# Kernel optimization log

Measured on AMD Instinct MI355X. Metric: run time of the kernel, lower is better.

Reference implementation:

```python
import jax, jax.numpy as jnp
import numpy as np

EPS = 1e-12  # matches torch F.normalize eps clamp


def _l2norm(v, axis):
    n = jnp.sqrt(jnp.sum(v * v, axis=axis, keepdims=True))
    return v / jnp.maximum(n, EPS)


def setup_inputs() -> dict:
    key = jax.random.key(0)
    k1, k2, k3, k4 = jax.random.split(key, 4)
    N, C, H, W, K = 64, 128, 64, 64, 64
    x = jax.random.normal(k1, (N, C, H, W), dtype=jnp.float32)
    conv_w = jax.random.normal(k2, (K, C), dtype=jnp.float32) * 0.1  # 1x1 conv weight squeezed
    conv_b = jax.random.normal(k3, (K,), dtype=jnp.float32) * 0.1
    centroids = jax.random.uniform(k4, (K, C), dtype=jnp.float32)
    return {"x": x, "conv_w": conv_w, "conv_b": conv_b, "centroids": centroids}


def reference(x, conv_w, conv_b, centroids):
    N, C = x.shape[:2]
    K = centroids.shape[0]
    xf = x.reshape(N, C, -1)                                   # (N, C, P) with P = H*W
    # 1x1 conv == per-pixel linear map over channels
    logits = jnp.einsum('ncp,kc->nkp', xf, conv_w) + conv_b[None, :, None]
    a = jax.nn.softmax(logits, axis=1)                         # soft assignment over clusters
    # vlad[n,k,c] = sum_p a[n,k,p] * (x[n,c,p] - centroids[k,c])
    vlad = jnp.einsum('nkp,ncp->nkc', a, xf) \
        - jnp.sum(a, axis=-1)[:, :, None] * centroids[None]    # (N, K, C)
    vlad = _l2norm(vlad, axis=2)                               # intra-cluster normalization
    vlad = vlad.reshape(N, K * C)
    return _l2norm(vlad, axis=1)
```

## Files before the change

kernel.cpp:

```cpp
#include <hip/hip_runtime.h>
#include <math.h>

#define NNIMG 64
#define CCH 128
#define KK 64
#define PP 4096
#define BSPLIT 16
#define PB (PP / BSPLIT)
#define PC 32
#define NCHUNK (PB / PC)

typedef __attribute__((ext_vector_type(8))) short short8;
typedef __attribute__((ext_vector_type(4))) float f32x4;

__device__ __forceinline__ unsigned short bf16_rtne(float f) {
  unsigned u = __float_as_uint(f);
  unsigned r = u + 0x7FFFu + ((u >> 16) & 1u);
  return (unsigned short)(r >> 16);
}
__device__ __forceinline__ float bf16_tof(unsigned short h) {
  return __uint_as_float(((unsigned)h) << 16);
}
__device__ __forceinline__ void lgkm_barrier() {
  __asm__ volatile("s_waitcnt lgkmcnt(0)\n\ts_barrier" ::: "memory");
}

template <bool USE_WS>
__global__ __launch_bounds__(128, 2) void netvlad_main(
    const float* __restrict__ x, const float* __restrict__ conv_w,
    const float* __restrict__ conv_b, const float* __restrict__ centroids,
    float* __restrict__ vout, float* __restrict__ aout) {
  __shared__ __align__(16) unsigned int pc[2][PC * 66];
  __shared__ __align__(16) unsigned short a_lds[KK * 40];
  __shared__ __align__(16) unsigned short w_lds[16 * 64 * 8];
  __shared__ float asum_buf[2 * KK];

  const int t = threadIdx.x;
  const int lane = t & 63;
  const int wv = t >> 6;
  const int m = lane & 15;
  const int q = lane >> 4;

  const int n = blockIdx.x / BSPLIT;
  const int blk = blockIdx.x % BSPLIT;
  const float* xbase = x + (size_t)n * CCH * PP + blk * PB;

  const int lrow = lane >> 3;
  const int lpx = (lane & 7) * 4;
  f32x4 sregA[8], sregB[8];
  auto issue_loads = [&](int ch, f32x4 (&sr)[8]) {
#pragma unroll
    for (int j = 0; j < 8; ++j) {
      const int row = wv * 64 + (j >> 1) * 16 + lrow * 2 + (j & 1);
      sr[j] = *(const f32x4*)(xbase + (size_t)row * PP + ch * PC + lpx);
    }
  };

  issue_loads(0, sregA);
  issue_loads(1, sregB);

#pragma unroll
  for (int kt = 0; kt < 4; ++kt)
#pragma unroll
    for (int cs = 0; cs < 4; ++cs) {
      const float* wp = conv_w + (kt * 16 + m) * CCH + cs * 32 + q * 8;
      float4 wa = *(const float4*)wp;
      float4 wb = *(const float4*)(wp + 4);
      float fv[8] = {wa.x, wa.y, wa.z, wa.w, wb.x, wb.y, wb.z, wb.w};
      short8 h;
#pragma unroll
      for (int j = 0; j < 8; ++j) h[j] = (short)bf16_rtne(fv[j]);
      *(short8*)&w_lds[(kt * 4 + cs) * 512 + lane * 8] = h;
    }
  float b_regs[4][4];
#pragma unroll
  for (int kt = 0; kt < 4; ++kt)
#pragma unroll
    for (int r = 0; r < 4; ++r) b_regs[kt][r] = conv_b[kt * 16 + q * 4 + r];

  f32x4 vacc[4][4];
#pragma unroll
  for (int kt = 0; kt < 4; ++kt)
#pragma unroll
    for (int ct = 0; ct < 4; ++ct) vacc[kt][ct] = (f32x4){0.f, 0.f, 0.f, 0.f};
  float asum_acc[16];
#pragma unroll
  for (int i = 0; i < 16; ++i) asum_acc[i] = 0.f;

  const int prow = wv * 16 + m;
  const unsigned sel_hi = 0x07060302u;
  const unsigned sel_g2 = (m & 1) ? 0x07060302u : 0x05040100u;

  auto chunk_body = [&](int ch, f32x4 (&sc)[8]) {
    unsigned int* pcb = pc[ch & 1];

#pragma unroll
    for (int u = 0; u < 4; ++u) {
      const int e = wv * 32 + u * 8 + lrow;
      f32x4 ev = sc[2 * u];
      f32x4 od = sc[2 * u + 1];
#pragma unroll
      for (int pi = 0; pi < 4; ++pi)
        pcb[(lpx + pi) * 66 + e] =
            __builtin_amdgcn_perm(__float_as_uint(od[pi]), __float_as_uint(ev[pi]), sel_hi);
    }
    if (ch + 2 < NCHUNK) issue_loads(ch + 2, sc);
    lgkm_barrier();

    f32x4 acc1[4];
#pragma unroll
    for (int kt = 0; kt < 4; ++kt)
      acc1[kt] = (f32x4){b_regs[kt][0], b_regs[kt][1], b_regs[kt][2], b_regs[kt][3]};
    const unsigned int* pcrow = pcb + prow * 66;
#pragma unroll
    for (int cs = 0; cs < 4; ++cs) {
      uint2 u01 = *(const uint2*)&pcrow[16 * cs + 4 * q];
      uint2 u23 = *(const uint2*)&pcrow[16 * cs + 4 * q + 2];
      unsigned hs[4] = {u01.x, u01.y, u23.x, u23.y};
      short8 Bf;
      __builtin_memcpy(&Bf, hs, 16);
#pragma unroll
      for (int kt = 0; kt < 4; ++kt) {
        short8 Wf = *(const short8*)&w_lds[(kt * 4 + cs) * 512 + lane * 8];
        acc1[kt] = __builtin_amdgcn_mfma_f32_16x16x32_bf16(Wf, Bf, acc1[kt], 0, 0, 0);
      }
    }

    float ssum = 0.f;
#pragma unroll
    for (int kt = 0; kt < 4; ++kt)
#pragma unroll
      for (int r = 0; r < 4; ++r) {
        float e = __expf(acc1[kt][r]);
        acc1[kt][r] = e;
        ssum += e;
      }
    ssum += __shfl_xor(ssum, 16, 64);
    ssum += __shfl_xor(ssum, 32, 64);
    float inv = 1.0f / ssum;
#pragma unroll
    for (int kt = 0; kt < 4; ++kt)
#pragma unroll
      for (int r = 0; r < 4; ++r) {
        float a = acc1[kt][r] * inv;
        unsigned short h = bf16_rtne(a);
        asum_acc[kt * 4 + r] += bf16_tof(h);
        a_lds[(kt * 16 + q * 4 + r) * 40 + prow] = h;
      }
    lgkm_barrier();

    short8 Af[4];
#pragma unroll
    for (int kt = 0; kt < 4; ++kt)
      Af[kt] = *(const short8*)&a_lds[(kt * 16 + m) * 40 + q * 8];
#pragma unroll
    for (int ct = 0; ct < 4; ++ct) {
      const int ebase = wv * 32 + ct * 8 + (m >> 1);
      unsigned g[8];
#pragma unroll
      for (int j = 0; j < 8; ++j) g[j] = pcb[(q * 8 + j) * 66 + ebase];
      unsigned hs2[4];
#pragma unroll
      for (int i = 0; i < 4; ++i)
        hs2[i] = __builtin_amdgcn_perm(g[2 * i + 1], g[2 * i], sel_g2);
      short8 Bf;
      __builtin_memcpy(&Bf, hs2, 16);
#pragma unroll
      for (int kt = 0; kt < 4; ++kt)
        vacc[kt][ct] = __builtin_amdgcn_mfma_f32_16x16x32_bf16(Af[kt], Bf, vacc[kt][ct], 0, 0, 0);
    }
  };

#pragma unroll 1
  for (int ch = 0; ch < NCHUNK; ch += 2) {
    chunk_body(ch, sregA);
    chunk_body(ch + 1, sregB);
  }

#pragma unroll
  for (int i = 0; i < 16; ++i) {
    float v = asum_acc[i];
    v += __shfl_xor(v, 1, 64);
    v += __shfl_xor(v, 2, 64);
    v += __shfl_xor(v, 4, 64);
    v += __shfl_xor(v, 8, 64);
    if (m == 0) asum_buf[wv * 64 + (i >> 2) * 16 + q * 4 + (i & 3)] = v;
  }
  lgkm_barrier();

  if (USE_WS) {
    float* vrow = vout + (size_t)blockIdx.x * (KK * CCH);
#pragma unroll
    for (int kt = 0; kt < 4; ++kt)
#pragma unroll
      for (int ct = 0; ct < 4; ++ct)
#pragma unroll
        for (int r = 0; r < 4; ++r) {
          const int idx = (kt * 16 + q * 4 + r) * CCH + wv * 64 + ct * 16 + m;
          vrow[idx] = vacc[kt][ct][r];
        }
    if (t < KK) aout[blockIdx.x * KK + t] = asum_buf[t] + asum_buf[KK + t];
  } else {
    float s_k[16];
#pragma unroll
    for (int i = 0; i < 16; ++i) {
      const int k = (i >> 2) * 16 + q * 4 + (i & 3);
      s_k[i] = asum_buf[k] + asum_buf[KK + k];
    }
    float* orow = vout + (size_t)n * (KK * CCH);
#pragma unroll
    for (int kt = 0; kt < 4; ++kt)
#pragma unroll
      for (int ct = 0; ct < 4; ++ct)
#pragma unroll
        for (int r = 0; r < 4; ++r) {
          const int k = kt * 16 + q * 4 + r;
          const int c = wv * 64 + ct * 16 + m;
          atomicAdd(&orow[k * CCH + c],
                    vacc[kt][ct][r] - s_k[kt * 4 + r] * centroids[k * CCH + c]);
        }
  }
}

__global__ __launch_bounds__(256) void netvlad_finish_ws(
    const float* __restrict__ vp, const float* __restrict__ agp,
    const float* __restrict__ centroids, float* __restrict__ out) {
  const int t = threadIdx.x;
  const int w = t >> 6, ln = t & 63;
  const int idx = blockIdx.x * 4 + w;
  const int n = idx >> 6, k = idx & 63;
  const int c = ln * 2;
  float a0 = 0.f, a1 = 0.f, s = 0.f;
#pragma unroll
  for (int b = 0; b < BSPLIT; ++b) {
    const float* vr = vp + (size_t)(n * BSPLIT + b) * (KK * CCH) + k * CCH + c;
    float2 v = *(const float2*)vr;
    a0 += v.x;
    a1 += v.y;
    s += agp[(n * BSPLIT + b) * KK + k];
  }
  float2 ce = *(const float2*)&centroids[k * CCH + c];
  float v0 = a0 - s * ce.x;
  float v1 = a1 - s * ce.y;
  float ssq = v0 * v0 + v1 * v1;
#pragma unroll
  for (int off = 32; off > 0; off >>= 1) ssq += __shfl_xor(ssq, off, 64);
  float inv = 0.125f / fmaxf(sqrtf(ssq), 1e-12f);
  float2 o;
  o.x = v0 * inv;
  o.y = v1 * inv;
  *(float2*)&out[(size_t)n * (KK * CCH) + k * CCH + c] = o;
}

__global__ __launch_bounds__(256) void netvlad_norm(float* __restrict__ out) {
  const int t = threadIdx.x;
  const int w = t >> 6, ln = t & 63;
  const int idx = blockIdx.x * 4 + w;
  float* vr = out + (size_t)idx * CCH;
  const int c = ln * 2;
  float2 v = *(const float2*)&vr[c];
  float ssq = v.x * v.x + v.y * v.y;
#pragma unroll
  for (int off = 32; off > 0; off >>= 1) ssq += __shfl_xor(ssq, off, 64);
  float inv = 0.125f / fmaxf(sqrtf(ssq), 1e-12f);
  float2 o;
  o.x = v.x * inv;
  o.y = v.y * inv;
  *(float2*)&vr[c] = o;
}

extern "C" void kernel_launch(void* const* d_in, const int* in_sizes, int n_in,
                              void* d_out, int out_size, void* d_ws, size_t ws_size,
                              hipStream_t stream) {
  const float* x = (const float*)d_in[0];
  const float* conv_w = (const float*)d_in[1];
  const float* conv_b = (const float*)d_in[2];
  const float* centroids = (const float*)d_in[3];
  float* out = (float*)d_out;

  const size_t WS_NEEDED =
      ((size_t)NNIMG * BSPLIT * KK * CCH + (size_t)NNIMG * BSPLIT * KK) * sizeof(float);

  if (ws_size >= WS_NEEDED) {
    float* vp = (float*)d_ws;
    float* agp = vp + (size_t)NNIMG * BSPLIT * KK * CCH;
    netvlad_main<true><<<NNIMG * BSPLIT, 128, 0, stream>>>(x, conv_w, conv_b,
                                                           centroids, vp, agp);
    netvlad_finish_ws<<<NNIMG * KK / 4, 256, 0, stream>>>(vp, agp, centroids, out);
  } else {
    hipMemsetAsync(d_out, 0, (size_t)NNIMG * KK * CCH * sizeof(float), stream);
    netvlad_main<false><<<NNIMG * BSPLIT, 128, 0, stream>>>(x, conv_w, conv_b,
                                                            centroids, out, nullptr);
    netvlad_norm<<<NNIMG * KK / 4, 256, 0, stream>>>(out);
  }
}
```

Before: 211.2 us.

## Stage 64-pixel chunks in a single LDS buffer with wider row loads

The x tile is now staged 64 pixels at a time in one LDS buffer instead of two 32-pixel double-buffered chunks, and each chunk is processed as two 32-pixel sub-chunks. The global load pattern changes to 16 lanes spanning 64 contiguous pixels per row, giving 256-byte contiguous row segments instead of 128-byte ones. The prefetch distance is now one 64-pixel chunk instead of two 32-pixel chunks. A single buffer adds an extra barrier after every sub-chunk, and the staging writes can no longer overlap with reads from the previous chunk.

Result: no change. 215.0 us (+1.8%).

```diff
diff --git a/kernel.cpp b/kernel.cpp
--- a/kernel.cpp
+++ b/kernel.cpp
@@ -7,8 +7,8 @@
 #define PP 4096
 #define BSPLIT 16
 #define PB (PP / BSPLIT)
-#define PC 32
-#define NCHUNK (PB / PC)
+#define CPW 64
+#define NCP (PB / CPW)
 
 typedef __attribute__((ext_vector_type(8))) short short8;
 typedef __attribute__((ext_vector_type(4))) float f32x4;
@@ -30,7 +30,7 @@
     const float* __restrict__ x, const float* __restrict__ conv_w,
     const float* __restrict__ conv_b, const float* __restrict__ centroids,
     float* __restrict__ vout, float* __restrict__ aout) {
-  __shared__ __align__(16) unsigned int pc[2][PC * 66];
+  __shared__ __align__(16) unsigned int pc[CPW * 66];
   __shared__ __align__(16) unsigned short a_lds[KK * 40];
   __shared__ __align__(16) unsigned short w_lds[16 * 64 * 8];
   __shared__ float asum_buf[2 * KK];
@@ -45,19 +45,17 @@
   const int blk = blockIdx.x % BSPLIT;
   const float* xbase = x + (size_t)n * CCH * PP + blk * PB;
 
-  const int lrow = lane >> 3;
-  const int lpx = (lane & 7) * 4;
-  f32x4 sregA[8], sregB[8];
-  auto issue_loads = [&](int ch, f32x4 (&sr)[8]) {
-#pragma unroll
-    for (int j = 0; j < 8; ++j) {
-      const int row = wv * 64 + (j >> 1) * 16 + lrow * 2 + (j & 1);
-      sr[j] = *(const f32x4*)(xbase + (size_t)row * PP + ch * PC + lpx);
+  f32x4 sregE[8], sregO[8];
+  auto issue_loads = [&](int cp) {
+#pragma unroll
+    for (int u = 0; u < 8; ++u) {
+      const float* pe = xbase + (size_t)(wv * 64 + u * 8 + 2 * q) * PP + cp * CPW + m * 4;
+      sregE[u] = *(const f32x4*)pe;
+      sregO[u] = *(const f32x4*)(pe + PP);
     }
   };
 
-  issue_loads(0, sregA);
-  issue_loads(1, sregB);
+  issue_loads(0);
 
 #pragma unroll
   for (int kt = 0; kt < 4; ++kt)
@@ -87,94 +85,92 @@
 #pragma unroll
   for (int i = 0; i < 16; ++i) asum_acc[i] = 0.f;
 
-  const int prow = wv * 16 + m;
   const unsigned sel_hi = 0x07060302u;
   const unsigned sel_g2 = (m & 1) ? 0x07060302u : 0x05040100u;
 
-  auto chunk_body = [&](int ch, f32x4 (&sc)[8]) {
-    unsigned int* pcb = pc[ch & 1];
-
-#pragma unroll
-    for (int u = 0; u < 4; ++u) {
-      const int e = wv * 32 + u * 8 + lrow;
-      f32x4 ev = sc[2 * u];
-      f32x4 od = sc[2 * u + 1];
+#pragma unroll 1
+  for (int cp = 0; cp < NCP; ++cp) {
+#pragma unroll
+    for (int u = 0; u < 8; ++u) {
+      const int e = wv * 32 + u * 4 + q;
+      f32x4 ev = sregE[u];
+      f32x4 od = sregO[u];
 #pragma unroll
       for (int pi = 0; pi < 4; ++pi)
-        pcb[(lpx + pi) * 66 + e] =
+        pc[(m * 4 + pi) * 66 + e] =
             __builtin_amdgcn_perm(__float_as_uint(od[pi]), __float_as_uint(ev[pi]), sel_hi);
     }
-    if (ch + 2 < NCHUNK) issue_loads(ch + 2, sc);
+    if (cp + 1 < NCP) issue_loads(cp + 1);
     lgkm_barrier();
 
-    f32x4 acc1[4];
-#pragma unroll
-    for (int kt = 0; kt < 4; ++kt)
-      acc1[kt] = (f32x4){b_regs[kt][0], b_regs[kt][1], b_regs[kt][2], b_regs[kt][3]};
-    const unsigned int* pcrow = pcb + prow * 66;
-#pragma unroll
-    for (int cs = 0; cs < 4; ++cs) {
-      uint2 u01 = *(const uint2*)&pcrow[16 * cs + 4 * q];
-      uint2 u23 = *(const uint2*)&pcrow[16 * cs + 4 * q + 2];
-      unsigned hs[4] = {u01.x, u01.y, u23.x, u23.y};
-      short8 Bf;
-      __builtin_memcpy(&Bf, hs, 16);
-#pragma unroll
-      for (int kt = 0; kt < 4; ++kt) {
-        short8 Wf = *(const short8*)&w_lds[(kt * 4 + cs) * 512 + lane * 8];
-        acc1[kt] = __builtin_amdgcn_mfma_f32_16x16x32_bf16(Wf, Bf, acc1[kt], 0, 0, 0);
+#pragma unroll
+    for (int sc = 0; sc < 2; ++sc) {
+      const int pxo = sc * 32;
+
+      f32x4 acc1[4];
+#pragma unroll
+      for (int kt = 0; kt < 4; ++kt)
+        acc1[kt] = (f32x4){b_regs[kt][0], b_regs[kt][1], b_regs[kt][2], b_regs[kt][3]};
+      const unsigned int* pcrow = pc + (pxo + wv * 16 + m) * 66;
+#pragma unroll
+      for (int cs = 0; cs < 4; ++cs) {
+        uint2 u01 = *(const uint2*)&pcrow[16 * cs + 4 * q];
+        uint2 u23 = *(const uint2*)&pcrow[16 * cs + 4 * q + 2];
+        unsigned hs[4] = {u01.x, u01.y, u23.x, u23.y};
+        short8 Bf;
+        __builtin_memcpy(&Bf, hs, 16);
+#pragma unroll
+        for (int kt = 0; kt < 4; ++kt) {
+          short8 Wf = *(const short8*)&w_lds[(kt * 4 + cs) * 512 + lane * 8];
+          acc1[kt] = __builtin_amdgcn_mfma_f32_16x16x32_bf16(Wf, Bf, acc1[kt], 0, 0, 0);
+        }
       }
-    }
-
-    float ssum = 0.f;
-#pragma unroll
-    for (int kt = 0; kt < 4; ++kt)
-#pragma unroll
-      for (int r = 0; r < 4; ++r) {
-        float e = __expf(acc1[kt][r]);
-        acc1[kt][r] = e;
-        ssum += e;
+
+      float ssum = 0.f;
+#pragma unroll
+      for (int kt = 0; kt < 4; ++kt)
+#pragma unroll
+        for (int r = 0; r < 4; ++r) {
+          float e = __expf(acc1[kt][r]);
+          acc1[kt][r] = e;
+          ssum += e;
+        }
+      ssum += __shfl_xor(ssum, 16, 64);
+      ssum += __shfl_xor(ssum, 32, 64);
+      float inv = 1.0f / ssum;
+#pragma unroll
+      for (int kt = 0; kt < 4; ++kt)
+#pragma unroll
+        for (int r = 0; r < 4; ++r) {
+          float a = acc1[kt][r] * inv;
+          unsigned short h = bf16_rtne(a);
+          asum_acc[kt * 4 + r] += bf16_tof(h);
+          a_lds[(kt * 16 + q * 4 + r) * 40 + wv * 16 + m] = h;
+        }
+      lgkm_barrier();
+
+      short8 Af[4];
+#pragma unroll
+      for (int kt = 0; kt < 4; ++kt)
+        Af[kt] = *(const short8*)&a_lds[(kt * 16 + m) * 40 + q * 8];
+#pragma unroll
+      for (int ct = 0; ct < 4; ++ct) {
+        const int ebase = wv * 32 + ct * 8 + (m >> 1);
+        unsigned g[8];
+#pragma unroll
+        for (int j = 0; j < 8; ++j) g[j] = pc[(pxo + q * 8 + j) * 66 + ebase];
+        unsigned hs2[4];
+#pragma unroll
+        for (int i = 0; i < 4; ++i)
+          hs2[i] = __builtin_amdgcn_perm(g[2 * i + 1], g[2 * i], sel_g2);
+        short8 Bf;
+        __builtin_memcpy(&Bf, hs2, 16);
+#pragma unroll
+        for (int kt = 0; kt < 4; ++kt)
+          vacc[kt][ct] = __builtin_amdgcn_mfma_f32_16x16x32_bf16(Af[kt], Bf, vacc[kt][ct], 0, 0, 0);
       }
-    ssum += __shfl_xor(ssum, 16, 64);
-    ssum += __shfl_xor(ssum, 32, 64);
-    float inv = 1.0f / ssum;
-#pragma unroll
-    for (int kt = 0; kt < 4; ++kt)
-#pragma unroll
-      for (int r = 0; r < 4; ++r) {
-        float a = acc1[kt][r] * inv;
-        unsigned short h = bf16_rtne(a);
-        asum_acc[kt * 4 + r] += bf16_tof(h);
-        a_lds[(kt * 16 + q * 4 + r) * 40 + prow] = h;
-      }
-    lgkm_barrier();
-
-    short8 Af[4];
-#pragma unroll
-    for (int kt = 0; kt < 4; ++kt)
-      Af[kt] = *(const short8*)&a_lds[(kt * 16 + m) * 40 + q * 8];
-#pragma unroll
-    for (int ct = 0; ct < 4; ++ct) {
-      const int ebase = wv * 32 + ct * 8 + (m >> 1);
-      unsigned g[8];
-#pragma unroll
-      for (int j = 0; j < 8; ++j) g[j] = pcb[(q * 8 + j) * 66 + ebase];
-      unsigned hs2[4];
-#pragma unroll
-      for (int i = 0; i < 4; ++i)
-        hs2[i] = __builtin_amdgcn_perm(g[2 * i + 1], g[2 * i], sel_g2);
-      short8 Bf;
-      __builtin_memcpy(&Bf, hs2, 16);
-#pragma unroll
-      for (int kt = 0; kt < 4; ++kt)
-        vacc[kt][ct] = __builtin_amdgcn_mfma_f32_16x16x32_bf16(Af[kt], Bf, vacc[kt][ct], 0, 0, 0);
-    }
-  };
-
-#pragma unroll 1
-  for (int ch = 0; ch < NCHUNK; ch += 2) {
-    chunk_body(ch, sregA);
-    chunk_body(ch + 1, sregB);
+      lgkm_barrier();
+    }
   }
 
 #pragma unroll
```
